# Performance work log

Measured on AMD Instinct MI355X. Metric: run time of the kernel, lower is better.

## Reference

```python
import jax, jax.numpy as jnp
import numpy as np

D = 768
H = 12
B, T = 2, 2048


def _layernorm(x, g, b, eps=1e-5):
    m = jnp.mean(x, axis=-1, keepdims=True)
    v = jnp.mean((x - m) ** 2, axis=-1, keepdims=True)
    return (x - m) * jax.lax.rsqrt(v + eps) * g + b


def setup_inputs() -> dict:
    key = jax.random.key(0)
    ks = jax.random.split(key, 10)
    s = 0.02
    return {
        "x": jax.random.normal(ks[0], (B, T, D), dtype=jnp.float32),
        "attn_mask": jnp.ones((B, T), dtype=jnp.int32),
        "Wq": jax.random.normal(ks[1], (D, D), dtype=jnp.float32) * s,
        "Wk": jax.random.normal(ks[2], (D, D), dtype=jnp.float32) * s,
        "Wv": jax.random.normal(ks[3], (D, D), dtype=jnp.float32) * s,
        "Wo": jax.random.normal(ks[4], (D, D), dtype=jnp.float32) * s,
        "bo": jnp.zeros((D,), dtype=jnp.float32),
        "ln1_g": jnp.ones((D,), dtype=jnp.float32),
        "ln1_b": jnp.zeros((D,), dtype=jnp.float32),
        "ln2_g": jnp.ones((D,), dtype=jnp.float32),
        "ln2_b": jnp.zeros((D,), dtype=jnp.float32),
        "W1": jax.random.normal(ks[5], (D, 4 * D), dtype=jnp.float32) * s,
        "b1": jnp.zeros((4 * D,), dtype=jnp.float32),
        "W2": jax.random.normal(ks[6], (4 * D, D), dtype=jnp.float32) * s,
        "b2": jnp.zeros((D,), dtype=jnp.float32),
    }


def reference(x, attn_mask, Wq, Wk, Wv, Wo, bo, ln1_g, ln1_b, ln2_g, ln2_b, W1, b1, W2, b2):
    d = x.shape[-1]
    hs = d // H
    # --- multi-head self-attention on ln1(x) ---
    h = _layernorm(x, ln1_g, ln1_b)
    q = jnp.einsum("btd,dhk->bhtk", h, Wq.reshape(d, H, hs))
    k = jnp.einsum("btd,dhk->bhtk", h, Wk.reshape(d, H, hs))
    v = jnp.einsum("btd,dhk->bhtk", h, Wv.reshape(d, H, hs))
    # NOTE: original scales by embed_dim**-0.5 (C = embed_dim), not head_size
    scores = jnp.einsum("bhtk,bhsk->bhts", q, k) * (d ** -0.5)
    key_mask = (attn_mask == 0)[:, None, None, :]  # [B,1,1,T] over key dim
    scores = jnp.where(key_mask, -jnp.inf, scores)
    wei = jax.nn.softmax(scores, axis=-1)
    out = jnp.einsum("bhts,bhsk->bhtk", wei, v)
    out = out.transpose(0, 2, 1, 3).reshape(x.shape)  # concat heads -> [B,T,D]
    x = x + out @ Wo + bo
    # --- feed-forward on ln2(x) ---
    h2 = _layernorm(x, ln2_g, ln2_b)
    ff = jax.nn.relu(h2 @ W1 + b1) @ W2 + b2
    return x + ff
```

## Files before the change

kernel.cpp:

```cpp
#include <hip/hip_runtime.h>
#include <hip/hip_bf16.h>


typedef unsigned short u16;
typedef unsigned int u32;
typedef __attribute__((ext_vector_type(8))) short s16x8;
typedef __attribute__((ext_vector_type(4))) short s16x4;
typedef __attribute__((ext_vector_type(4))) float fx4;

#define D_MODEL 768
#define NH 12
#define HS 64
#define TT 2048
#define BB 2

__device__ __forceinline__ u16 f2bf(float f) {
  union { float f; u32 u; } v; v.f = f;
  u32 r = v.u + 0x7fffu + ((v.u >> 16) & 1u);
  return (u16)(r >> 16);
}
__device__ __forceinline__ float bf2f(u16 h) {
  union { u32 u; float f; } v; v.u = ((u32)h) << 16; return v.f;
}
__device__ __forceinline__ s16x4 pack4(float a, float b, float c, float d) {
  union { __hip_bfloat162 h2[2]; s16x4 v; } u;
  u.h2[0] = __float22bfloat162_rn({a, b});
  u.h2[1] = __float22bfloat162_rn({c, d});
  return u.v;
}

__device__ __forceinline__ void async16(const void* g, void* l) {
  __builtin_amdgcn_global_load_lds(
      (const __attribute__((address_space(1))) u32*)g,
      (__attribute__((address_space(3))) u32*)l, 16, 0, 0);
}

__global__ __launch_bounds__(256) void tconv(const float* __restrict__ in,
                                             u16* __restrict__ out, int R, int C) {
  __shared__ float t[32][33];
  int c0 = blockIdx.x * 32, r0 = blockIdx.y * 32;
  int x = threadIdx.x, y = threadIdx.y;
  for (int i = 0; i < 4; i++)
    t[y + i * 8][x] = in[(size_t)(r0 + y + i * 8) * C + c0 + x];
  __syncthreads();
  for (int i = 0; i < 4; i++)
    out[(size_t)(c0 + y + i * 8) * R + r0 + x] = f2bf(t[x][y + i * 8]);
}

__global__ __launch_bounds__(256) void tconv3(const float* __restrict__ w0,
                                              const float* __restrict__ w1,
                                              const float* __restrict__ w2,
                                              u16* __restrict__ out) {
  __shared__ float t[32][33];
  const float* in = blockIdx.z == 0 ? w0 : blockIdx.z == 1 ? w1 : w2;
  u16* o = out + (size_t)blockIdx.z * 768 * 768;
  int c0 = blockIdx.x * 32, r0 = blockIdx.y * 32;
  int x = threadIdx.x, y = threadIdx.y;
  for (int i = 0; i < 4; i++)
    t[y + i * 8][x] = in[(size_t)(r0 + y + i * 8) * 768 + c0 + x];
  __syncthreads();
  for (int i = 0; i < 4; i++)
    o[(size_t)(c0 + y + i * 8) * 768 + r0 + x] = f2bf(t[x][y + i * 8]);
}

__global__ __launch_bounds__(256) void vt_extract(const u16* __restrict__ qkv,
                                                  u16* __restrict__ vt) {
  __shared__ u16 t[32][33];
  int bh = blockIdx.z, b = bh / NH, h = bh % NH;
  int t0 = blockIdx.x * 32, v0 = blockIdx.y * 32;
  int x = threadIdx.x, y = threadIdx.y;
  for (int i = 0; i < 4; i++)
    t[y + i * 8][x] = qkv[(size_t)(b * TT + t0 + y + i * 8) * 2304 + 1536 + h * HS + v0 + x];
  __syncthreads();
  for (int i = 0; i < 4; i++)
    vt[(size_t)(bh * HS + v0 + y + i * 8) * TT + t0 + x] = t[x][y + i * 8];
}

__global__ __launch_bounds__(256) void maskbias(const int* __restrict__ mask,
                                                float* __restrict__ mb) {
  int i = blockIdx.x * 256 + threadIdx.x;
  mb[i] = mask[i] ? 0.f : -1e30f;
}

__global__ __launch_bounds__(256) void ln_kernel(const float* __restrict__ x,
                                                 const float* __restrict__ g,
                                                 const float* __restrict__ bta,
                                                 u16* __restrict__ out) {
  int row = blockIdx.x;
  const float* xr = x + (size_t)row * D_MODEL;
  int tid = threadIdx.x;
  float v0 = xr[tid], v1 = xr[tid + 256], v2 = xr[tid + 512];
  float s = v0 + v1 + v2, sq = v0 * v0 + v1 * v1 + v2 * v2;
  for (int m = 1; m < 64; m <<= 1) { s += __shfl_xor(s, m); sq += __shfl_xor(sq, m); }
  __shared__ float ss[4], ssq[4];
  int w = tid >> 6;
  if ((tid & 63) == 0) { ss[w] = s; ssq[w] = sq; }
  __syncthreads();
  s = ss[0] + ss[1] + ss[2] + ss[3];
  sq = ssq[0] + ssq[1] + ssq[2] + ssq[3];
  float mean = s * (1.f / D_MODEL);
  float var = sq * (1.f / D_MODEL) - mean * mean;
  float rstd = rsqrtf(var + 1e-5f);
  u16* orow = out + (size_t)row * D_MODEL;
  orow[tid]       = f2bf((v0 - mean) * rstd * g[tid]       + bta[tid]);
  orow[tid + 256] = f2bf((v1 - mean) * rstd * g[tid + 256] + bta[tid + 256]);
  orow[tid + 512] = f2bf((v2 - mean) * rstd * g[tid + 512] + bta[tid + 512]);
}

__global__ __launch_bounds__(256) void red_wo_ln(
    const u16* __restrict__ p0, const u16* __restrict__ p1,
    const u16* __restrict__ p2, const u16* __restrict__ p3,
    const float* __restrict__ x, const float* __restrict__ bo,
    const float* __restrict__ g, const float* __restrict__ be,
    float* __restrict__ yv, u16* __restrict__ h2) {
  int row = blockIdx.x, tid = threadIdx.x;
  size_t base = (size_t)row * D_MODEL;
  float v[3];
  float s = 0.f, sq = 0.f;
  for (int i = 0; i < 3; i++) {
    int c = tid + i * 256;
    size_t idx = base + c;
    float t = bf2f(p0[idx]) + bf2f(p1[idx]) + bf2f(p2[idx]) + bf2f(p3[idx])
            + x[idx] + bo[c];
    v[i] = t; yv[idx] = t;
    s += t; sq += t * t;
  }
  for (int m = 1; m < 64; m <<= 1) { s += __shfl_xor(s, m); sq += __shfl_xor(sq, m); }
  __shared__ float ss[4], ssq[4];
  int w = tid >> 6;
  if ((tid & 63) == 0) { ss[w] = s; ssq[w] = sq; }
  __syncthreads();
  s = ss[0] + ss[1] + ss[2] + ss[3];
  sq = ssq[0] + ssq[1] + ssq[2] + ssq[3];
  float mean = s * (1.f / D_MODEL);
  float var = sq * (1.f / D_MODEL) - mean * mean;
  float rstd = rsqrtf(var + 1e-5f);
  for (int i = 0; i < 3; i++) {
    int c = tid + i * 256;
    h2[base + c] = f2bf((v[i] - mean) * rstd * g[c] + be[c]);
  }
}

__global__ __launch_bounds__(256) void red_ff2(
    const u16* __restrict__ p0, const u16* __restrict__ p1,
    const u16* __restrict__ p2, const float* __restrict__ yv,
    const float* __restrict__ bias, float* __restrict__ out) {
  size_t i = ((size_t)blockIdx.x * 256 + threadIdx.x) * 4;
  int col = (int)(i % D_MODEL);
  ushort4 a = *(const ushort4*)(p0 + i);
  ushort4 b = *(const ushort4*)(p1 + i);
  ushort4 c = *(const ushort4*)(p2 + i);
  float4 y = *(const float4*)(yv + i);
  float4 o;
  o.x = bf2f(a.x) + bf2f(b.x) + bf2f(c.x) + y.x + bias[col];
  o.y = bf2f(a.y) + bf2f(b.y) + bf2f(c.y) + y.y + bias[col + 1];
  o.z = bf2f(a.z) + bf2f(b.z) + bf2f(c.z) + y.z + bias[col + 2];
  o.w = bf2f(a.w) + bf2f(b.w) + bf2f(c.w) + y.w + bias[col + 3];
  *(float4*)(out + i) = o;
}

template <int EPI>
__global__ __launch_bounds__(256) void gemm_bt(
    const u16* __restrict__ A, const u16* __restrict__ Bt,
    int M, int N, int K,
    u16* __restrict__ outb, const float* __restrict__ bias,
    float qs, int qn,
    u16* __restrict__ p0, u16* __restrict__ p1,
    u16* __restrict__ p2, u16* __restrict__ p3) {
  __shared__ __align__(16) u16 lA[128 * 32];
  __shared__ __align__(16) u16 lB[128 * 32];
  const int tid = threadIdx.x;
  const int lane = tid & 63, w = tid >> 6;
  const int quad = lane >> 4, l15 = lane & 15;
  const int wm = w >> 1, wn = w & 1;
  const int bm = blockIdx.y, bn = blockIdx.x;
  const int Ksub = K / gridDim.z;
  const int k0 = blockIdx.z * Ksub;

  fx4 acc[4][4] = {};

  for (int kt = k0; kt < k0 + Ksub; kt += 32) {
    __syncthreads();
    for (int t = 0; t < 2; t++) {
      int p = (w * 2 + t) * 64 + lane;
      int m = p >> 2, qp = p & 3;
      int ql = qp ^ ((m >> 1) & 3);
      async16(A + (size_t)(bm * 128 + m) * K + kt + ql * 8,
              (char*)lA + (w * 2 + t) * 1024);
    }
    for (int t = 0; t < 2; t++) {
      int p = (w * 2 + t) * 64 + lane;
      int n = p >> 2, qp = p & 3;
      int ql = qp ^ ((n >> 1) & 3);
      async16(Bt + (size_t)(bn * 128 + n) * K + kt + ql * 8,
              (char*)lB + (w * 2 + t) * 1024);
    }
    __syncthreads();
    s16x8 af[4], bfr[4];
    for (int i = 0; i < 4; i++) {
      int m = wm * 64 + i * 16 + l15;
      int phys = m * 4 + (quad ^ ((m >> 1) & 3));
      af[i] = *(const s16x8*)((const char*)lA + phys * 16);
    }
    for (int j = 0; j < 4; j++) {
      int n = wn * 64 + j * 16 + l15;
      int phys = n * 4 + (quad ^ ((n >> 1) & 3));
      bfr[j] = *(const s16x8*)((const char*)lB + phys * 16);
    }
    for (int i = 0; i < 4; i++)
      for (int j = 0; j < 4; j++)
        acc[i][j] = __builtin_amdgcn_mfma_f32_16x16x32_bf16(af[i], bfr[j], acc[i][j], 0, 0, 0);
  }

  u16* pb = nullptr;
  if (EPI == 3)
    pb = blockIdx.z == 0 ? p0 : blockIdx.z == 1 ? p1 : blockIdx.z == 2 ? p2 : p3;

  for (int i = 0; i < 4; i++)
    for (int j = 0; j < 4; j++)
      for (int r = 0; r < 4; r++) {
        int row = bm * 128 + wm * 64 + i * 16 + quad * 4 + r;
        int col = bn * 128 + wn * 64 + j * 16 + l15;
        float v = acc[i][j][r];
        if (EPI == 0) {
          float vv = (col < qn) ? v * qs : v;
          outb[(size_t)row * N + col] = f2bf(vv);
        } else if (EPI == 2) {
          outb[(size_t)row * N + col] = f2bf(fmaxf(v + bias[col], 0.f));
        } else {
          pb[(size_t)row * N + col] = f2bf(v);
        }
      }
}

__global__ __launch_bounds__(512) void attn_kernel(
    const u16* __restrict__ qkv, const u16* __restrict__ vt,
    const float* __restrict__ maskadd,
    u16* __restrict__ pO0, u16* __restrict__ pO1, float* __restrict__ pL) {
  __shared__ __align__(16) u16 sQ[128 * 64];
  __shared__ __align__(16) u16 sK[64 * 64];
  __shared__ __align__(16) u16 sV[64 * 68];
  __shared__ __align__(16) float smask[1024];
  const int bh = blockIdx.y, b = bh / NH, h = bh % NH;
  const int qt = blockIdx.x, sp = blockIdx.z;
  const int tid = threadIdx.x, lane = tid & 63, w = tid >> 6;
  const int quad = lane >> 4, l15 = lane & 15;

  for (int i = 0; i < 2; i++) {
    int p = i * 512 + tid;
    int m = p >> 3, qp = p & 7, ql = qp ^ (m & 7);
    async16(qkv + (size_t)(b * TT + qt * 128 + m) * 2304 + h * HS + ql * 8,
            (char*)sQ + i * 8192 + w * 1024);
  }
  smask[tid]       = maskadd[b * TT + sp * 1024 + tid];
  smask[tid + 512] = maskadd[b * TT + sp * 1024 + 512 + tid];
  const u16* vbase = vt + (size_t)bh * HS * TT + (size_t)(tid >> 3) * TT + sp * 1024;
  s16x8 vcur = *(const s16x8*)(vbase + (tid & 7) * 8);
  __syncthreads();

  const int qrow = w * 16 + l15;
  s16x8 aq0 = *(const s16x8*)((const char*)sQ + qrow * 128 + ((quad ^ (l15 & 7)) * 16));
  s16x8 aq1 = *(const s16x8*)((const char*)sQ + qrow * 128 + (((4 + quad) ^ (l15 & 7)) * 16));

  const char* pK0 = (const char*)sK + l15 * 128 + ((quad ^ (l15 & 7)) * 16);
  const char* pK1 = (const char*)sK + l15 * 128 + (((4 + quad) ^ (l15 & 7)) * 16);
  const char* pV  = (const char*)sV + l15 * 136 + quad * 8;
  char* vwr = (char*)sV + (tid >> 3) * 136 + (tid & 7) * 16;

  float lsum = 0.f;
  fx4 o[4] = {};

  for (int kc = 0; kc < 16; kc++) {
    __syncthreads();
    {
      int m = tid >> 3, qp = tid & 7, ql = qp ^ (m & 7);
      async16(qkv + (size_t)(b * TT + sp * 1024 + kc * 64 + m) * 2304 + D_MODEL + h * HS + ql * 8,
              (char*)sK + w * 1024);
    }
    *(s16x8*)vwr = vcur;
    __syncthreads();
    int kn = (kc < 15) ? (kc + 1) * 64 : kc * 64;
    s16x8 vnxt = *(const s16x8*)(vbase + kn + (tid & 7) * 8);

    #pragma unroll
    for (int kt = 0; kt < 4; kt++) {
      float4 mb = *(const float4*)&smask[kc * 64 + kt * 16 + quad * 4];
      fx4 s = {mb.x, mb.y, mb.z, mb.w};
      s16x8 ak0 = *(const s16x8*)(pK0 + kt * 2048);
      s16x8 ak1 = *(const s16x8*)(pK1 + kt * 2048);
      s = __builtin_amdgcn_mfma_f32_16x16x32_bf16(ak0, aq0, s, 0, 0, 0);
      s = __builtin_amdgcn_mfma_f32_16x16x32_bf16(ak1, aq1, s, 0, 0, 0);
      float e0 = __builtin_amdgcn_exp2f(s[0]);
      float e1 = __builtin_amdgcn_exp2f(s[1]);
      float e2 = __builtin_amdgcn_exp2f(s[2]);
      float e3 = __builtin_amdgcn_exp2f(s[3]);
      lsum += (e0 + e1) + (e2 + e3);
      s16x4 pB = pack4(e0, e1, e2, e3);
      #pragma unroll
      for (int jv = 0; jv < 4; jv++) {
        s16x4 av = *(const s16x4*)(pV + jv * 2176 + kt * 32);
        o[jv] = __builtin_amdgcn_mfma_f32_16x16x16bf16_1k(av, pB, o[jv], 0, 0, 0);
      }
    }
    vcur = vnxt;
  }

  lsum += __shfl_xor(lsum, 16);
  lsum += __shfl_xor(lsum, 32);

  const int tile = bh * 32 + qt * 2 + (w >> 2);
  const int sub = (w & 3) * 16;
  u16* po = sp ? pO1 : pO0;
  size_t base = (size_t)tile * 4096;
  for (int jv = 0; jv < 4; jv++)
    for (int r = 0; r < 4; r++) {
      int vd = jv * 16 + quad * 4 + r;
      po[base + vd * 64 + sub + l15] = f2bf(o[jv][r]);
    }
  if (quad == 0) pL[sp * 49152 + tile * 64 + sub + l15] = lsum;
}

__global__ __launch_bounds__(256) void attn_reduce(
    const u16* __restrict__ pO0, const u16* __restrict__ pO1,
    const float* __restrict__ pL, u16* __restrict__ out) {
  __shared__ float T[64 * 65];
  __shared__ float rinv[64];
  const int tile = blockIdx.x;
  const int bh = tile >> 5, qt = tile & 31, b = bh / NH, h = bh % NH;
  const int t = threadIdx.x;
  if (t < 64) rinv[t] = 1.f / (pL[tile * 64 + t] + pL[49152 + tile * 64 + t]);
  __syncthreads();
  size_t base = (size_t)tile * 4096;
  for (int i = 0; i < 16; i++) {
    int idx = i * 256 + t, vd = idx >> 6, q = idx & 63;
    T[vd * 65 + q] = (bf2f(pO0[base + idx]) + bf2f(pO1[base + idx])) * rinv[q];
  }
  __syncthreads();
  int q = t >> 2, vb = (t & 3) * 16;
  u16* orow = out + (size_t)(b * TT + qt * 64 + q) * D_MODEL + h * HS + vb;
  for (int i = 0; i < 8; i++) {
    int vd = vb + i * 2;
    u32 pk = (u32)f2bf(T[vd * 65 + q]) | ((u32)f2bf(T[(vd + 1) * 65 + q]) << 16);
    *(u32*)(orow + i * 2) = pk;
  }
}

extern "C" void kernel_launch(void* const* d_in, const int* in_sizes, int n_in,
                              void* d_out, int out_size, void* d_ws, size_t ws_size,
                              hipStream_t stream) {
  const float* x    = (const float*)d_in[0];
  const int*   mask = (const int*)d_in[1];
  const float* Wq   = (const float*)d_in[2];
  const float* Wk   = (const float*)d_in[3];
  const float* Wv   = (const float*)d_in[4];
  const float* Wo   = (const float*)d_in[5];
  const float* bo   = (const float*)d_in[6];
  const float* g1   = (const float*)d_in[7];
  const float* be1  = (const float*)d_in[8];
  const float* g2   = (const float*)d_in[9];
  const float* be2  = (const float*)d_in[10];
  const float* W1   = (const float*)d_in[11];
  const float* bb1  = (const float*)d_in[12];
  const float* W2   = (const float*)d_in[13];
  const float* bb2  = (const float*)d_in[14];
  float* out = (float*)d_out;
  char* ws = (char*)d_ws;

  u16*   WqkvT = (u16*)(ws + 0);
  u16*   WoT   = (u16*)(ws + 3538944);
  u16*   W1T   = (u16*)(ws + 4718592);
  u16*   W2T   = (u16*)(ws + 9437184);
  u16*   h1    = (u16*)(ws + 14155776);
  u16*   QKV   = (u16*)(ws + 20447232);
  u16*   Vt    = (u16*)(ws + 39321600);
  u16*   attn  = (u16*)(ws + 45613056);
  float* yv    = (float*)(ws + 51904512);
  float* mbias = yv;
  u16*   pO0   = h1;
  u16*   pO1   = (u16*)(ws + 51920896);
  float* pL    = (float*)(ws + 58212352);
  u16*   h2    = h1;
  u16*   ff1   = QKV;
  u16* pw0 = (u16*)(ws + 20447232);
  u16* pw1 = (u16*)(ws + 26738688);
  u16* pw2 = (u16*)(ws + 33030144);
  u16* pw3 = (u16*)(ws + 39321600);
  u16* pf0 = (u16*)(ws + 0);
  u16* pf1 = (u16*)(ws + 14155776);
  u16* pf2 = (u16*)(ws + 45613056);

  const float QS = 0.05205875399f;

  dim3 tb(32, 8);
  tconv3<<<dim3(24, 24, 3), tb, 0, stream>>>(Wq, Wk, Wv, WqkvT);
  tconv<<<dim3(24, 24), tb, 0, stream>>>(Wo, WoT, 768, 768);
  tconv<<<dim3(96, 24), tb, 0, stream>>>(W1, W1T, 768, 3072);
  tconv<<<dim3(24, 96), tb, 0, stream>>>(W2, W2T, 3072, 768);
  maskbias<<<16, 256, 0, stream>>>(mask, mbias);

  ln_kernel<<<4096, 256, 0, stream>>>(x, g1, be1, h1);
  gemm_bt<0><<<dim3(18, 32, 1), 256, 0, stream>>>(h1, WqkvT, 4096, 2304, 768,
      QKV, nullptr, QS, 768, nullptr, nullptr, nullptr, nullptr);
  vt_extract<<<dim3(64, 2, 24), tb, 0, stream>>>(QKV, Vt);
  attn_kernel<<<dim3(16, 24, 2), 512, 0, stream>>>(QKV, Vt, mbias, pO0, pO1, pL);
  attn_reduce<<<768, 256, 0, stream>>>(pO0, pO1, pL, attn);
  gemm_bt<3><<<dim3(6, 32, 4), 256, 0, stream>>>(attn, WoT, 4096, 768, 768,
      nullptr, nullptr, 1.f, 0, pw0, pw1, pw2, pw3);
  red_wo_ln<<<4096, 256, 0, stream>>>(pw0, pw1, pw2, pw3, x, bo, g2, be2, yv, h2);
  gemm_bt<2><<<dim3(24, 32, 1), 256, 0, stream>>>(h2, W1T, 4096, 3072, 768,
      ff1, bb1, 1.f, 0, nullptr, nullptr, nullptr, nullptr);
  gemm_bt<3><<<dim3(6, 32, 3), 256, 0, stream>>>(ff1, W2T, 4096, 768, 3072,
      nullptr, nullptr, 1.f, 0, pf0, pf1, pf2, nullptr);
  red_ff2<<<3072, 256, 0, stream>>>(pf0, pf1, pf2, yv, bb2, out);
}
```

Baseline: 301.8 us.

## Fuse preprocessing kernels, write V transposed from QKV GEMM, deepen GEMM K-tile

Merges the weight transposes, LN1, and mask-bias kernels into one launch to cut launch overhead. The QKV GEMM epilogue now writes the V columns directly in transposed layout, which removes the separate vt_extract pass over QKV. The GEMM K step grows from 32 to 64 with a new 8-way XOR swizzle, halving barrier count per K. In exchange the GEMMs use twice the LDS, and the V columns are no longer written into QKV, so attention must read V only from Vt.

```diff
diff --git a/kernel.cpp b/kernel.cpp
--- a/kernel.cpp
+++ b/kernel.cpp
@@ -35,76 +35,63 @@
       (__attribute__((address_space(3))) u32*)l, 16, 0, 0);
 }
 
-__global__ __launch_bounds__(256) void tconv(const float* __restrict__ in,
-                                             u16* __restrict__ out, int R, int C) {
+__global__ __launch_bounds__(256) void preproc(
+    const float* __restrict__ x, const int* __restrict__ mask,
+    const float* __restrict__ Wq, const float* __restrict__ Wk,
+    const float* __restrict__ Wv, const float* __restrict__ Wo,
+    const float* __restrict__ W1, const float* __restrict__ W2,
+    const float* __restrict__ g1, const float* __restrict__ be1,
+    u16* __restrict__ WqkvT, u16* __restrict__ WoT,
+    u16* __restrict__ W1T, u16* __restrict__ W2T,
+    u16* __restrict__ h1, float* __restrict__ mb) {
   __shared__ float t[32][33];
-  int c0 = blockIdx.x * 32, r0 = blockIdx.y * 32;
-  int x = threadIdx.x, y = threadIdx.y;
-  for (int i = 0; i < 4; i++)
-    t[y + i * 8][x] = in[(size_t)(r0 + y + i * 8) * C + c0 + x];
-  __syncthreads();
-  for (int i = 0; i < 4; i++)
-    out[(size_t)(c0 + y + i * 8) * R + r0 + x] = f2bf(t[x][y + i * 8]);
-}
-
-__global__ __launch_bounds__(256) void tconv3(const float* __restrict__ w0,
-                                              const float* __restrict__ w1,
-                                              const float* __restrict__ w2,
-                                              u16* __restrict__ out) {
-  __shared__ float t[32][33];
-  const float* in = blockIdx.z == 0 ? w0 : blockIdx.z == 1 ? w1 : w2;
-  u16* o = out + (size_t)blockIdx.z * 768 * 768;
-  int c0 = blockIdx.x * 32, r0 = blockIdx.y * 32;
-  int x = threadIdx.x, y = threadIdx.y;
-  for (int i = 0; i < 4; i++)
-    t[y + i * 8][x] = in[(size_t)(r0 + y + i * 8) * 768 + c0 + x];
-  __syncthreads();
-  for (int i = 0; i < 4; i++)
-    o[(size_t)(c0 + y + i * 8) * 768 + r0 + x] = f2bf(t[x][y + i * 8]);
-}
-
-__global__ __launch_bounds__(256) void vt_extract(const u16* __restrict__ qkv,
-                                                  u16* __restrict__ vt) {
-  __shared__ u16 t[32][33];
-  int bh = blockIdx.z, b = bh / NH, h = bh % NH;
-  int t0 = blockIdx.x * 32, v0 = blockIdx.y * 32;
-  int x = threadIdx.x, y = threadIdx.y;
-  for (int i = 0; i < 4; i++)
-    t[y + i * 8][x] = qkv[(size_t)(b * TT + t0 + y + i * 8) * 2304 + 1536 + h * HS + v0 + x];
-  __syncthreads();
-  for (int i = 0; i < 4; i++)
-    vt[(size_t)(bh * HS + v0 + y + i * 8) * TT + t0 + x] = t[x][y + i * 8];
-}
-
-__global__ __launch_bounds__(256) void maskbias(const int* __restrict__ mask,
-                                                float* __restrict__ mb) {
-  int i = blockIdx.x * 256 + threadIdx.x;
-  mb[i] = mask[i] ? 0.f : -1e30f;
-}
-
-__global__ __launch_bounds__(256) void ln_kernel(const float* __restrict__ x,
-                                                 const float* __restrict__ g,
-                                                 const float* __restrict__ bta,
-                                                 u16* __restrict__ out) {
-  int row = blockIdx.x;
-  const float* xr = x + (size_t)row * D_MODEL;
-  int tid = threadIdx.x;
-  float v0 = xr[tid], v1 = xr[tid + 256], v2 = xr[tid + 512];
-  float s = v0 + v1 + v2, sq = v0 * v0 + v1 * v1 + v2 * v2;
-  for (int m = 1; m < 64; m <<= 1) { s += __shfl_xor(s, m); sq += __shfl_xor(sq, m); }
   __shared__ float ss[4], ssq[4];
-  int w = tid >> 6;
-  if ((tid & 63) == 0) { ss[w] = s; ssq[w] = sq; }
-  __syncthreads();
-  s = ss[0] + ss[1] + ss[2] + ss[3];
-  sq = ssq[0] + ssq[1] + ssq[2] + ssq[3];
-  float mean = s * (1.f / D_MODEL);
-  float var = sq * (1.f / D_MODEL) - mean * mean;
-  float rstd = rsqrtf(var + 1e-5f);
-  u16* orow = out + (size_t)row * D_MODEL;
-  orow[tid]       = f2bf((v0 - mean) * rstd * g[tid]       + bta[tid]);
-  orow[tid + 256] = f2bf((v1 - mean) * rstd * g[tid + 256] + bta[tid + 256]);
-  orow[tid + 512] = f2bf((v2 - mean) * rstd * g[tid + 512] + bta[tid + 512]);
+  const int bid = blockIdx.x, tid = threadIdx.x;
+  if (bid < 6912) {
+    const float* in; u16* out; int R, C, cx, cy;
+    if (bid < 1728) {
+      int wsel = bid / 576, s = bid % 576;
+      in = wsel == 0 ? Wq : wsel == 1 ? Wk : Wv;
+      out = WqkvT + (size_t)wsel * 768 * 768;
+      R = 768; C = 768; cx = s % 24; cy = s / 24;
+    } else if (bid < 2304) {
+      int s = bid - 1728; in = Wo; out = WoT;
+      R = 768; C = 768; cx = s % 24; cy = s / 24;
+    } else if (bid < 4608) {
+      int s = bid - 2304; in = W1; out = W1T;
+      R = 768; C = 3072; cx = s % 96; cy = s / 96;
+    } else {
+      int s = bid - 4608; in = W2; out = W2T;
+      R = 3072; C = 768; cx = s % 24; cy = s / 24;
+    }
+    int c0 = cx * 32, r0 = cy * 32, xx = tid & 31, yy = tid >> 5;
+    for (int i = 0; i < 4; i++)
+      t[yy + i * 8][xx] = in[(size_t)(r0 + yy + i * 8) * C + c0 + xx];
+    __syncthreads();
+    for (int i = 0; i < 4; i++)
+      out[(size_t)(c0 + yy + i * 8) * R + r0 + xx] = f2bf(t[xx][yy + i * 8]);
+  } else if (bid < 11008) {
+    int row = bid - 6912;
+    const float* xr = x + (size_t)row * D_MODEL;
+    float v0 = xr[tid], v1 = xr[tid + 256], v2 = xr[tid + 512];
+    float s = v0 + v1 + v2, sq = v0 * v0 + v1 * v1 + v2 * v2;
+    for (int m = 1; m < 64; m <<= 1) { s += __shfl_xor(s, m); sq += __shfl_xor(sq, m); }
+    int w = tid >> 6;
+    if ((tid & 63) == 0) { ss[w] = s; ssq[w] = sq; }
+    __syncthreads();
+    s = ss[0] + ss[1] + ss[2] + ss[3];
+    sq = ssq[0] + ssq[1] + ssq[2] + ssq[3];
+    float mean = s * (1.f / D_MODEL);
+    float var = sq * (1.f / D_MODEL) - mean * mean;
+    float rstd = rsqrtf(var + 1e-5f);
+    u16* orow = h1 + (size_t)row * D_MODEL;
+    orow[tid]       = f2bf((v0 - mean) * rstd * g1[tid]       + be1[tid]);
+    orow[tid + 256] = f2bf((v1 - mean) * rstd * g1[tid + 256] + be1[tid + 256]);
+    orow[tid + 512] = f2bf((v2 - mean) * rstd * g1[tid + 512] + be1[tid + 512]);
+  } else {
+    int i = (bid - 11008) * 256 + tid;
+    mb[i] = mask[i] ? 0.f : -1e30f;
+  }
 }
 
 __global__ __launch_bounds__(256) void red_wo_ln(
@@ -164,11 +151,11 @@
     const u16* __restrict__ A, const u16* __restrict__ Bt,
     int M, int N, int K,
     u16* __restrict__ outb, const float* __restrict__ bias,
-    float qs, int qn,
+    float qs, u16* __restrict__ vtp,
     u16* __restrict__ p0, u16* __restrict__ p1,
     u16* __restrict__ p2, u16* __restrict__ p3) {
-  __shared__ __align__(16) u16 lA[128 * 32];
-  __shared__ __align__(16) u16 lB[128 * 32];
+  __shared__ __align__(16) u16 lA[128 * 64];
+  __shared__ __align__(16) u16 lB[128 * 64];
   const int tid = threadIdx.x;
   const int lane = tid & 63, w = tid >> 6;
   const int quad = lane >> 4, l15 = lane & 15;
@@ -179,58 +166,75 @@
 
   fx4 acc[4][4] = {};
 
-  for (int kt = k0; kt < k0 + Ksub; kt += 32) {
-    __syncthreads();
-    for (int t = 0; t < 2; t++) {
-      int p = (w * 2 + t) * 64 + lane;
-      int m = p >> 2, qp = p & 3;
-      int ql = qp ^ ((m >> 1) & 3);
+  for (int kt = k0; kt < k0 + Ksub; kt += 64) {
+    __syncthreads();
+    #pragma unroll
+    for (int t = 0; t < 4; t++) {
+      int p = t * 256 + tid;
+      int m = p >> 3, qp = p & 7, ql = qp ^ (m & 7);
       async16(A + (size_t)(bm * 128 + m) * K + kt + ql * 8,
-              (char*)lA + (w * 2 + t) * 1024);
-    }
-    for (int t = 0; t < 2; t++) {
-      int p = (w * 2 + t) * 64 + lane;
-      int n = p >> 2, qp = p & 3;
-      int ql = qp ^ ((n >> 1) & 3);
+              (char*)lA + t * 4096 + w * 1024);
+    }
+    #pragma unroll
+    for (int t = 0; t < 4; t++) {
+      int p = t * 256 + tid;
+      int n = p >> 3, qp = p & 7, ql = qp ^ (n & 7);
       async16(Bt + (size_t)(bn * 128 + n) * K + kt + ql * 8,
-              (char*)lB + (w * 2 + t) * 1024);
-    }
-    __syncthreads();
-    s16x8 af[4], bfr[4];
-    for (int i = 0; i < 4; i++) {
-      int m = wm * 64 + i * 16 + l15;
-      int phys = m * 4 + (quad ^ ((m >> 1) & 3));
-      af[i] = *(const s16x8*)((const char*)lA + phys * 16);
-    }
-    for (int j = 0; j < 4; j++) {
-      int n = wn * 64 + j * 16 + l15;
-      int phys = n * 4 + (quad ^ ((n >> 1) & 3));
-      bfr[j] = *(const s16x8*)((const char*)lB + phys * 16);
-    }
-    for (int i = 0; i < 4; i++)
-      for (int j = 0; j < 4; j++)
-        acc[i][j] = __builtin_amdgcn_mfma_f32_16x16x32_bf16(af[i], bfr[j], acc[i][j], 0, 0, 0);
+              (char*)lB + t * 4096 + w * 1024);
+    }
+    __syncthreads();
+    #pragma unroll
+    for (int kk = 0; kk < 2; kk++) {
+      s16x8 af[4], bfr[4];
+      #pragma unroll
+      for (int i = 0; i < 4; i++) {
+        int m = wm * 64 + i * 16 + l15;
+        af[i] = *(const s16x8*)((const char*)lA + m * 128 +
+                                (((kk * 4 + quad) ^ (m & 7)) * 16));
+      }
+      #pragma unroll
+      for (int j = 0; j < 4; j++) {
+        int n = wn * 64 + j * 16 + l15;
+        bfr[j] = *(const s16x8*)((const char*)lB + n * 128 +
+                                 (((kk * 4 + quad) ^ (n & 7)) * 16));
+      }
+      #pragma unroll
+      for (int i = 0; i < 4; i++)
+        #pragma unroll
+        for (int j = 0; j < 4; j++)
+          acc[i][j] = __builtin_amdgcn_mfma_f32_16x16x32_bf16(af[i], bfr[j], acc[i][j], 0, 0, 0);
+    }
   }
 
   u16* pb = nullptr;
   if (EPI == 3)
     pb = blockIdx.z == 0 ? p0 : blockIdx.z == 1 ? p1 : blockIdx.z == 2 ? p2 : p3;
 
+  #pragma unroll
   for (int i = 0; i < 4; i++)
-    for (int j = 0; j < 4; j++)
-      for (int r = 0; r < 4; r++) {
-        int row = bm * 128 + wm * 64 + i * 16 + quad * 4 + r;
-        int col = bn * 128 + wn * 64 + j * 16 + l15;
-        float v = acc[i][j][r];
-        if (EPI == 0) {
-          float vv = (col < qn) ? v * qs : v;
-          outb[(size_t)row * N + col] = f2bf(vv);
-        } else if (EPI == 2) {
-          outb[(size_t)row * N + col] = f2bf(fmaxf(v + bias[col], 0.f));
+    #pragma unroll
+    for (int j = 0; j < 4; j++) {
+      int row0 = bm * 128 + wm * 64 + i * 16 + quad * 4;
+      int col = bn * 128 + wn * 64 + j * 16 + l15;
+      if (EPI == 0) {
+        if (vtp != nullptr && col >= 1536) {
+          int bb = row0 >> 11, t0 = row0 & 2047;
+          ushort4 pk = {f2bf(acc[i][j][0]), f2bf(acc[i][j][1]),
+                        f2bf(acc[i][j][2]), f2bf(acc[i][j][3])};
+          *(ushort4*)(vtp + ((size_t)(bb * 768 + (col - 1536)) << 11) + t0) = pk;
         } else {
-          pb[(size_t)row * N + col] = f2bf(v);
+          float sc = (col < 768) ? qs : 1.f;
+          for (int r = 0; r < 4; r++)
+            outb[(size_t)(row0 + r) * N + col] = f2bf(acc[i][j][r] * sc);
         }
+      } else if (EPI == 2) {
+        for (int r = 0; r < 4; r++)
+          outb[(size_t)(row0 + r) * N + col] = f2bf(fmaxf(acc[i][j][r] + bias[col], 0.f));
+      } else {
+        for (int r = 0; r < 4; r++)
+          pb[(size_t)(row0 + r) * N + col] = f2bf(acc[i][j][r]);
       }
+    }
 }
 
 __global__ __launch_bounds__(512) void attn_kernel(
@@ -391,25 +395,18 @@
 
   const float QS = 0.05205875399f;
 
-  dim3 tb(32, 8);
-  tconv3<<<dim3(24, 24, 3), tb, 0, stream>>>(Wq, Wk, Wv, WqkvT);
-  tconv<<<dim3(24, 24), tb, 0, stream>>>(Wo, WoT, 768, 768);
-  tconv<<<dim3(96, 24), tb, 0, stream>>>(W1, W1T, 768, 3072);
-  tconv<<<dim3(24, 96), tb, 0, stream>>>(W2, W2T, 3072, 768);
-  maskbias<<<16, 256, 0, stream>>>(mask, mbias);
-
-  ln_kernel<<<4096, 256, 0, stream>>>(x, g1, be1, h1);
+  preproc<<<11024, 256, 0, stream>>>(x, mask, Wq, Wk, Wv, Wo, W1, W2,
+                                     g1, be1, WqkvT, WoT, W1T, W2T, h1, mbias);
   gemm_bt<0><<<dim3(18, 32, 1), 256, 0, stream>>>(h1, WqkvT, 4096, 2304, 768,
-      QKV, nullptr, QS, 768, nullptr, nullptr, nullptr, nullptr);
-  vt_extract<<<dim3(64, 2, 24), tb, 0, stream>>>(QKV, Vt);
+      QKV, nullptr, QS, Vt, nullptr, nullptr, nullptr, nullptr);
   attn_kernel<<<dim3(16, 24, 2), 512, 0, stream>>>(QKV, Vt, mbias, pO0, pO1, pL);
   attn_reduce<<<768, 256, 0, stream>>>(pO0, pO1, pL, attn);
   gemm_bt<3><<<dim3(6, 32, 4), 256, 0, stream>>>(attn, WoT, 4096, 768, 768,
-      nullptr, nullptr, 1.f, 0, pw0, pw1, pw2, pw3);
+      nullptr, nullptr, 1.f, nullptr, pw0, pw1, pw2, pw3);
   red_wo_ln<<<4096, 256, 0, stream>>>(pw0, pw1, pw2, pw3, x, bo, g2, be2, yv, h2);
   gemm_bt<2><<<dim3(24, 32, 1), 256, 0, stream>>>(h2, W1T, 4096, 3072, 768,
-      ff1, bb1, 1.f, 0, nullptr, nullptr, nullptr, nullptr);
+      ff1, bb1, 1.f, nullptr, nullptr, nullptr, nullptr, nullptr);
   gemm_bt<3><<<dim3(6, 32, 3), 256, 0, stream>>>(ff1, W2T, 4096, 768, 3072,
-      nullptr, nullptr, 1.f, 0, pf0, pf1, pf2, nullptr);
+      nullptr, nullptr, 1.f, nullptr, pf0, pf1, pf2, nullptr);
   red_ff2<<<3072, 256, 0, stream>>>(pf0, pf1, pf2, yv, bb2, out);
 }
```

New measurement: 277.4 us. 8.1% less time.
